# Performance work log

Hardware: AMD Instinct MI355X
Metric: run time of the kernel (lower is better)

Reference implementation:

```python
import jax, jax.numpy as jnp
import numpy as np

NUM_HEADS = 16

def setup_inputs() -> dict:
    key = jax.random.key(0)
    ks = jax.random.split(key, 8)
    B, S, X, D = 2, 2048, 1, 1024
    scale = 1.0 / np.sqrt(D)
    return {
        "query": jax.random.normal(ks[0], (B, S, X, D), jnp.float32),
        "key": jax.random.normal(ks[1], (B, S, X, D), jnp.float32),
        "value": jax.random.normal(ks[2], (B, S, X, D), jnp.float32),
        "Wq": jax.random.normal(ks[3], (D, D), jnp.float32) * scale,
        "bq": jnp.zeros((D,), jnp.float32),
        "Wk": jax.random.normal(ks[4], (D, D), jnp.float32) * scale,
        "bk": jnp.zeros((D,), jnp.float32),
        "Wv": jax.random.normal(ks[5], (D, D), jnp.float32) * scale,
        "bv": jnp.zeros((D,), jnp.float32),
        "Wo": jax.random.normal(ks[6], (D, D), jnp.float32) * scale,
        "bo": jnp.zeros((D,), jnp.float32),
    }

def _split_heads(x, B, H):
    # [B, S, X, D] -> [B, H, S*X, depth]
    D = x.shape[-1]
    return x.reshape(B, -1, H, D // H).transpose(0, 2, 1, 3)

def reference(query, key, value, Wq, bq, Wk, bk, Wv, bv, Wo, bo):
    B, S, X, D = query.shape
    H = NUM_HEADS
    q = _split_heads(query @ Wq + bq, B, H)   # [B,H,L,dh], L=S*X
    k = _split_heads(key @ Wk + bk, B, H)
    v = _split_heads(value @ Wv + bv, B, H)
    dh = k.shape[-1]
    logits = jnp.einsum("bhqd,bhkd->bhqk", q, k) / jnp.sqrt(jnp.float32(dh))
    attn = jax.nn.softmax(logits, axis=-1)
    out = jnp.einsum("bhqk,bhkd->bhqd", attn, v)   # [B,H,L,dh]
    out = out.transpose(0, 2, 1, 3).reshape(B, S, -1, D)  # [B,S,X,D]
    return out @ Wo + bo
```

## Files before the change

### kernel.cpp

```cpp
#include <hip/hip_runtime.h>
#include <cstdint>
#include <cstddef>

typedef __bf16 bf16x8 __attribute__((ext_vector_type(8)));
typedef float f32x4 __attribute__((ext_vector_type(4)));
typedef float f32x16 __attribute__((ext_vector_type(16)));
typedef unsigned short u16;
typedef unsigned int u32;

static constexpr int Bn = 2;
static constexpr int L  = 2048;
static constexpr int Dm = 1024;
static constexpr int H  = 16;
static constexpr int DH = 64;
static constexpr int M  = Bn * L;

#define SC 0.18033688f

__device__ __forceinline__ u16 f2bf(float f) {
    union { float f; u32 u; } v; v.f = f;
    u32 u = v.u + 0x7FFFu + ((v.u >> 16) & 1u);
    return (u16)(u >> 16);
}

__device__ __forceinline__ u32 pk_bf16(float a, float b) {
#if __has_builtin(__builtin_amdgcn_cvt_pk_bf16_f32)
    typedef __bf16 bf16x2_t __attribute__((ext_vector_type(2)));
    bf16x2_t t = __builtin_amdgcn_cvt_pk_bf16_f32(a, b);
    u32 r; __builtin_memcpy(&r, &t, 4); return r;
#else
    return (u32)f2bf(a) | ((u32)f2bf(b) << 16);
#endif
}
__device__ __forceinline__ u16 f2bf1(float f) { return (u16)(pk_bf16(f, f) & 0xffffu); }

__device__ __forceinline__ void gl2lds16(const void* g, void* l) {
    __builtin_amdgcn_global_load_lds(
        (const __attribute__((address_space(1))) u32*)(uintptr_t)g,
        (__attribute__((address_space(3))) u32*)(uintptr_t)l, 16, 0, 0);
}

__global__ __launch_bounds__(256) void convert_in(
    const float* __restrict__ q, const float* __restrict__ k, const float* __restrict__ v,
    u16* __restrict__ dst)
{
    const float* src = (blockIdx.y == 0) ? q : (blockIdx.y == 1) ? k : v;
    u16* d = dst + (size_t)blockIdx.y * M * Dm;
    const size_t t = (size_t)blockIdx.x * 256 + threadIdx.x;
    const float4* s4 = reinterpret_cast<const float4*>(src) + t * 2;
    float4 f0 = s4[0], f1 = s4[1];
    u32 o[4] = { pk_bf16(f0.x, f0.y), pk_bf16(f0.z, f0.w),
                 pk_bf16(f1.x, f1.y), pk_bf16(f1.z, f1.w) };
    reinterpret_cast<uint4*>(d)[t] = *reinterpret_cast<uint4*>(o);
}

__global__ __launch_bounds__(256) void convert_wt(
    const float* __restrict__ Wq, const float* __restrict__ Wk,
    const float* __restrict__ Wv, const float* __restrict__ Wo,
    u16* __restrict__ dst)
{
    __shared__ u16 Ts[64][72];
    const int z = blockIdx.z;
    const float* W = (z == 0) ? Wq : (z == 1) ? Wk : (z == 2) ? Wv : Wo;
    u16* o = dst + (size_t)z * Dm * Dm;
    const int n0 = blockIdx.x * 64, k0 = blockIdx.y * 64;
    const int tid = threadIdx.x;

    {
        const int kr = tid >> 2, nc = (tid & 3) * 16;
        const float* s = W + (size_t)(k0 + kr) * Dm + n0 + nc;
        const float4* s4 = reinterpret_cast<const float4*>(s);
        float4 a = s4[0], b = s4[1], c = s4[2], d = s4[3];
        u32 t[8] = { pk_bf16(a.x, a.y), pk_bf16(a.z, a.w), pk_bf16(b.x, b.y), pk_bf16(b.z, b.w),
                     pk_bf16(c.x, c.y), pk_bf16(c.z, c.w), pk_bf16(d.x, d.y), pk_bf16(d.z, d.w) };
        *reinterpret_cast<uint4*>(&Ts[kr][nc])     = reinterpret_cast<uint4*>(t)[0];
        *reinterpret_cast<uint4*>(&Ts[kr][nc + 8]) = reinterpret_cast<uint4*>(t)[1];
    }
    __syncthreads();
    {
        const int nr = tid >> 2, kc = (tid & 3) * 16;
        u16 w[16];
        #pragma unroll
        for (int j = 0; j < 16; ++j) w[j] = Ts[kc + j][nr];
        u16* dptr = o + (size_t)(n0 + nr) * Dm + k0 + kc;
        *reinterpret_cast<uint4*>(dptr)     = reinterpret_cast<uint4*>(w)[0];
        *reinterpret_cast<uint4*>(dptr + 8) = reinterpret_cast<uint4*>(w)[1];
    }
}

__global__ __launch_bounds__(256) void gemm_qkv(
    const u16* __restrict__ Abuf, const u16* __restrict__ Wtb,
    const float* __restrict__ bq, const float* __restrict__ bk, const float* __restrict__ bv,
    u16* __restrict__ Qh, u16* __restrict__ Kh, u16* __restrict__ Vh)
{
    __shared__ u16 As[2][128 * 32];
    __shared__ u16 Bs[2][128 * 32];
    const int tid = threadIdx.x;
    const int wave = tid >> 6, lane = tid & 63;
    const int quad = lane >> 4, l16 = lane & 15;
    const int wr = wave >> 1, wc = wave & 1;
    const int z = blockIdx.z;
    const u16* A  = Abuf + (size_t)z * M * Dm;
    const u16* Bt = Wtb  + (size_t)z * Dm * Dm;
    const float* bias = (z == 0) ? bq : (z == 1) ? bk : bv;
    u16* out = (z == 0) ? Qh : (z == 1) ? Kh : Vh;
    const int n0 = blockIdx.x * 128, m0 = blockIdx.y * 128;

    const int srow = lane >> 2;
    const int skc  = (lane & 3) * 8;

    f32x4 acc[4][4] = {};

    auto stage = [&](int k0, int bi) {
        #pragma unroll
        for (int i = 0; i < 2; ++i) {
            const int ra = i * 64 + wave * 16;
            gl2lds16(A  + (size_t)(m0 + ra + srow) * Dm + k0 + skc, &As[bi][ra * 32]);
            gl2lds16(Bt + (size_t)(n0 + ra + srow) * Dm + k0 + skc, &Bs[bi][ra * 32]);
        }
    };

    stage(0, 0);
    for (int k0 = 0, it = 0; k0 < Dm; k0 += 32, ++it) {
        const int cb = it & 1;
        __syncthreads();
        if (k0 + 32 < Dm) stage(k0 + 32, cb ^ 1);
        bf16x8 af[4], bf[4];
        #pragma unroll
        for (int t = 0; t < 4; ++t) {
            af[t] = *reinterpret_cast<const bf16x8*>(&As[cb][(wr * 64 + t * 16 + l16) * 32 + quad * 8]);
            bf[t] = *reinterpret_cast<const bf16x8*>(&Bs[cb][(wc * 64 + t * 16 + l16) * 32 + quad * 8]);
        }
        #pragma unroll
        for (int mt = 0; mt < 4; ++mt)
            #pragma unroll
            for (int nt = 0; nt < 4; ++nt)
                acc[mt][nt] = __builtin_amdgcn_mfma_f32_16x16x32_bf16(af[mt], bf[nt], acc[mt][nt], 0, 0, 0);
    }

    const float qscale = (z == 0) ? SC : 1.0f;
    #pragma unroll
    for (int nt = 0; nt < 4; ++nt) {
        const int n = n0 + wc * 64 + nt * 16 + l16;
        const float badd = bias[n];
        const int h = n >> 6, d = n & 63;
        #pragma unroll
        for (int mt = 0; mt < 4; ++mt) {
            #pragma unroll
            for (int r = 0; r < 4; ++r) {
                const int m = m0 + wr * 64 + mt * 16 + quad * 4 + r;
                const int bb = m >> 11, ll = m & 2047;
                out[(((size_t)(bb * H + h)) * L + ll) * DH + d] = f2bf1((acc[mt][nt][r] + badd) * qscale);
            }
        }
    }
}

__global__ __launch_bounds__(256) void transpose_v(
    const u16* __restrict__ Vh, u16* __restrict__ Vth)
{
    __shared__ u16 Ts[64][72];
    const int kt = blockIdx.x, h = blockIdx.y, b = blockIdx.z;
    const int tid = threadIdx.x;
    const size_t hb = ((size_t)(b * H + h)) * L * DH;

    {
        const int kr = tid >> 2, dc = (tid & 3) * 16;
        const u16* s = Vh + hb + (size_t)(kt * 64 + kr) * DH + dc;
        *reinterpret_cast<uint4*>(&Ts[kr][dc])     = *reinterpret_cast<const uint4*>(s);
        *reinterpret_cast<uint4*>(&Ts[kr][dc + 8]) = *reinterpret_cast<const uint4*>(s + 8);
    }
    __syncthreads();
    {
        const int dr = tid >> 2, kc = (tid & 3) * 16;
        u16 w[16];
        #pragma unroll
        for (int j = 0; j < 16; ++j) w[j] = Ts[kc + j][dr];
        u16* dptr = Vth + hb + (size_t)dr * L + kt * 64 + kc;
        *reinterpret_cast<uint4*>(dptr)     = reinterpret_cast<uint4*>(w)[0];
        *reinterpret_cast<uint4*>(dptr + 8) = reinterpret_cast<uint4*>(w)[1];
    }
}

__global__ __launch_bounds__(256) void attn(
    const u16* __restrict__ Qh, const u16* __restrict__ Kh,
    const u16* __restrict__ Vth, u16* __restrict__ ctx)
{
    __shared__ __align__(16) char smem[32768];
    u16* Os = (u16*)smem;

    const int tid  = threadIdx.x;
    const int wave = tid >> 6, lane = tid & 63;
    const int l31  = lane & 31, hh = lane >> 5;
    const int qt = blockIdx.x, h = blockIdx.y, b = blockIdx.z;
    const size_t hb = ((size_t)(b * H + h)) * L * DH;
    const int q0 = qt * 128 + wave * 32;

    bf16x8 qf[4];
    {
        const u16* qp = Qh + hb + (size_t)(q0 + l31) * DH + hh * 8;
        #pragma unroll
        for (int c = 0; c < 4; ++c)
            qf[c] = *reinterpret_cast<const bf16x8*>(qp + c * 16);
    }

    const int r_off = lane >> 3;
    const int s_sl  = lane & 7;

    auto stage = [&](int kt, int bi) {
        char* base = smem + bi * 16384;
        #pragma unroll
        for (int i = 0; i < 2; ++i) {
            const int rr = wave * 16 + i * 8 + r_off;
            gl2lds16(Kh  + hb + (size_t)(kt * 64 + rr) * DH + ((s_sl ^ (rr & 7)) << 3),
                     base + (wave * 16 + i * 8) * 128);
            gl2lds16(Vth + hb + (size_t)rr * L + kt * 64 + ((s_sl ^ (rr & 7)) << 3),
                     base + 8192 + (wave * 16 + i * 8) * 128);
        }
    };

    int vbK[2], vbV[2];
    #pragma unroll
    for (int t = 0; t < 2; ++t) {
        const int rr = t * 32 + l31;
        vbK[t] = rr * 128 + ((rr & 7) << 4);
        vbV[t] = 8192 + rr * 128 + ((rr & 7) << 4);
    }

    float rsum = 0.f;
    f32x16 oacc[2] = {};

    stage(0, 0);
    for (int kt = 0; kt < L / 64; ++kt) {
        const int cb = kt & 1;
        __syncthreads();
        if (kt + 1 < L / 64) stage(kt + 1, cb ^ 1);
        const char* ldsb = smem + cb * 16384;

        f32x16 st[2] = {};
        #pragma unroll
        for (int t = 0; t < 2; ++t) {
            #pragma unroll
            for (int c = 0; c < 4; ++c) {
                bf16x8 kf = *reinterpret_cast<const bf16x8*>(ldsb + (vbK[t] ^ (((c << 1) | hh) << 4)));
                st[t] = __builtin_amdgcn_mfma_f32_32x32x16_bf16(kf, qf[c], st[t], 0, 0, 0);
            }
        }

        bf16x8 pfrag[4];
        #pragma unroll
        for (int t = 0; t < 2; ++t) {
            float p[16];
            #pragma unroll
            for (int rr = 0; rr < 16; ++rr) {
                p[rr] = __builtin_amdgcn_exp2f(st[t][rr]);
                rsum += p[rr];
            }
            #pragma unroll
            for (int g = 0; g < 2; ++g) {
                float* pg = p + g * 8;
                #pragma unroll
                for (int j = 0; j < 4; ++j)
                    asm volatile("v_permlane32_swap_b32 %0, %1" : "+v"(pg[j]), "+v"(pg[j + 4]));
                u32 pkv[4];
                #pragma unroll
                for (int j = 0; j < 4; ++j) pkv[j] = pk_bf16(pg[2 * j], pg[2 * j + 1]);
                pfrag[t * 2 + g] = *reinterpret_cast<bf16x8*>(pkv);
            }
        }

        #pragma unroll
        for (int t = 0; t < 2; ++t) {
            #pragma unroll
            for (int c = 0; c < 4; ++c) {
                bf16x8 vf = *reinterpret_cast<const bf16x8*>(ldsb + (vbV[t] ^ (((c << 1) | hh) << 4)));
                oacc[t] = __builtin_amdgcn_mfma_f32_32x32x16_bf16(vf, pfrag[c], oacc[t], 0, 0, 0);
            }
        }
    }

    rsum += __shfl_xor(rsum, 32);
    const float inv = 1.0f / rsum;

    #pragma unroll
    for (int pass = 0; pass < 2; ++pass) {
        __syncthreads();
        if ((wave >> 1) == pass) {
            const int qloc = (wave & 1) * 32 + l31;
            #pragma unroll
            for (int t = 0; t < 2; ++t) {
                #pragma unroll
                for (int rq = 0; rq < 4; ++rq) {
                    const int d0 = t * 32 + rq * 8 + hh * 4;
                    *reinterpret_cast<u32*>(&Os[qloc * 72 + d0]) =
                        pk_bf16(oacc[t][rq * 4 + 0] * inv, oacc[t][rq * 4 + 1] * inv);
                    *reinterpret_cast<u32*>(&Os[qloc * 72 + d0 + 2]) =
                        pk_bf16(oacc[t][rq * 4 + 2] * inv, oacc[t][rq * 4 + 3] * inv);
                }
            }
        }
        __syncthreads();
        {
            const int row = tid >> 2, cc = (tid & 3) * 16;
            u16* dst = ctx + ((size_t)(b * L + qt * 128 + pass * 64 + row)) * Dm + h * 64 + cc;
            *reinterpret_cast<uint4*>(dst)     = *reinterpret_cast<const uint4*>(&Os[row * 72 + cc]);
            *reinterpret_cast<uint4*>(dst + 8) = *reinterpret_cast<const uint4*>(&Os[row * 72 + cc + 8]);
        }
    }
}

__global__ __launch_bounds__(256) void gemm_out(
    const u16* __restrict__ A, const u16* __restrict__ Bt,
    const float* __restrict__ bias, float* __restrict__ out)
{
    __shared__ u16 As[2][128 * 32];
    __shared__ u16 Bs[2][64 * 32];
    const int tid = threadIdx.x;
    const int wave = tid >> 6, lane = tid & 63;
    const int quad = lane >> 4, l16 = lane & 15;
    const int n0 = blockIdx.x * 64, m0 = blockIdx.y * 128;

    const int srow = lane >> 2;
    const int skc  = (lane & 3) * 8;

    f32x4 acc[2][4] = {};

    auto stage = [&](int k0, int bi) {
        #pragma unroll
        for (int i = 0; i < 2; ++i) {
            const int ra = i * 64 + wave * 16;
            gl2lds16(A + (size_t)(m0 + ra + srow) * Dm + k0 + skc, &As[bi][ra * 32]);
        }
        gl2lds16(Bt + (size_t)(n0 + wave * 16 + srow) * Dm + k0 + skc, &Bs[bi][wave * 16 * 32]);
    };

    stage(0, 0);
    for (int k0 = 0, it = 0; k0 < Dm; k0 += 32, ++it) {
        const int cb = it & 1;
        __syncthreads();
        if (k0 + 32 < Dm) stage(k0 + 32, cb ^ 1);
        bf16x8 af[2], bf[4];
        #pragma unroll
        for (int t = 0; t < 2; ++t)
            af[t] = *reinterpret_cast<const bf16x8*>(&As[cb][(wave * 32 + t * 16 + l16) * 32 + quad * 8]);
        #pragma unroll
        for (int t = 0; t < 4; ++t)
            bf[t] = *reinterpret_cast<const bf16x8*>(&Bs[cb][(t * 16 + l16) * 32 + quad * 8]);
        #pragma unroll
        for (int mt = 0; mt < 2; ++mt)
            #pragma unroll
            for (int nt = 0; nt < 4; ++nt)
                acc[mt][nt] = __builtin_amdgcn_mfma_f32_16x16x32_bf16(af[mt], bf[nt], acc[mt][nt], 0, 0, 0);
    }

    #pragma unroll
    for (int nt = 0; nt < 4; ++nt) {
        const int n = n0 + nt * 16 + l16;
        const float badd = bias[n];
        #pragma unroll
        for (int mt = 0; mt < 2; ++mt) {
            #pragma unroll
            for (int r = 0; r < 4; ++r) {
                const int m = m0 + wave * 32 + mt * 16 + quad * 4 + r;
                out[(size_t)m * Dm + n] = acc[mt][nt][r] + badd;
            }
        }
    }
}

extern "C" void kernel_launch(void* const* d_in, const int* in_sizes, int n_in,
                              void* d_out, int out_size, void* d_ws, size_t ws_size,
                              hipStream_t stream) {
    const float* q  = (const float*)d_in[0];
    const float* k  = (const float*)d_in[1];
    const float* v  = (const float*)d_in[2];
    const float* Wq = (const float*)d_in[3];
    const float* bq = (const float*)d_in[4];
    const float* Wk = (const float*)d_in[5];
    const float* bk = (const float*)d_in[6];
    const float* Wv = (const float*)d_in[7];
    const float* bv = (const float*)d_in[8];
    const float* Wo = (const float*)d_in[9];
    const float* bo = (const float*)d_in[10];
    float* out = (float*)d_out;

    const size_t per = (size_t)Bn * H * L * DH;
    u16* Abuf = (u16*)d_ws;
    u16* Wt   = Abuf + 3 * (size_t)M * Dm;
    u16* Qh   = Wt + 4 * (size_t)Dm * Dm;
    u16* Kh   = Qh + per;
    u16* Vh   = Kh + per;
    u16* Vth  = Vh + per;
    u16* ctx  = Abuf;

    convert_in <<<dim3((M * Dm) / 8 / 256, 3), 256, 0, stream>>>(q, k, v, Abuf);
    convert_wt <<<dim3(Dm / 64, Dm / 64, 4), 256, 0, stream>>>(Wq, Wk, Wv, Wo, Wt);
    gemm_qkv   <<<dim3(Dm / 128, M / 128, 3), 256, 0, stream>>>(Abuf, Wt, bq, bk, bv, Qh, Kh, Vh);
    transpose_v<<<dim3(L / 64, H, Bn), 256, 0, stream>>>(Vh, Vth);
    attn       <<<dim3(L / 128, H, Bn), 256, 0, stream>>>(Qh, Kh, Vth, ctx);
    gemm_out   <<<dim3(Dm / 64, M / 128), 256, 0, stream>>>(ctx, Wt + 3 * (size_t)Dm * Dm, bo, out);
}
```

Measured before the change: 237.8 us.

## Split attention over key halves with merge kernel; fuse V transpose into QKV epilogue

The QKV GEMM epilogue now stages each wave's output tile in shared memory and writes Q/K rows and a transposed V with coalesced 16-byte stores. This removes the separate transpose_v kernel and its extra pass over V. The attention kernel now splits the key range in two, doubling the block count so the GPU is better occupied. Each half writes unnormalized partial outputs and row sums, and a new merge kernel adds the halves and normalizes. The merge costs an extra launch and extra global traffic for the partials. Summing the halves directly is only correct because the softmax does not subtract a running max.

```diff
diff --git a/kernel.cpp b/kernel.cpp
--- a/kernel.cpp
+++ b/kernel.cpp
@@ -14,6 +14,8 @@
 static constexpr int H  = 16;
 static constexpr int DH = 64;
 static constexpr int M  = Bn * L;
+static constexpr size_t PER = (size_t)Bn * H * L * DH;
+static constexpr int NQ = Bn * H * L;
 
 #define SC 0.18033688f
 
@@ -91,10 +93,10 @@
 __global__ __launch_bounds__(256) void gemm_qkv(
     const u16* __restrict__ Abuf, const u16* __restrict__ Wtb,
     const float* __restrict__ bq, const float* __restrict__ bk, const float* __restrict__ bv,
-    u16* __restrict__ Qh, u16* __restrict__ Kh, u16* __restrict__ Vh)
-{
-    __shared__ u16 As[2][128 * 32];
-    __shared__ u16 Bs[2][128 * 32];
+    u16* __restrict__ Qh, u16* __restrict__ Kh, u16* __restrict__ Vth)
+{
+    __shared__ __align__(16) char smem[36864];
+
     const int tid = threadIdx.x;
     const int wave = tid >> 6, lane = tid & 63;
     const int quad = lane >> 4, l16 = lane & 15;
@@ -103,7 +105,7 @@
     const u16* A  = Abuf + (size_t)z * M * Dm;
     const u16* Bt = Wtb  + (size_t)z * Dm * Dm;
     const float* bias = (z == 0) ? bq : (z == 1) ? bk : bv;
-    u16* out = (z == 0) ? Qh : (z == 1) ? Kh : Vh;
+    u16* out = (z == 0) ? Qh : (z == 1) ? Kh : Vth;
     const int n0 = blockIdx.x * 128, m0 = blockIdx.y * 128;
 
     const int srow = lane >> 2;
@@ -115,8 +117,8 @@
         #pragma unroll
         for (int i = 0; i < 2; ++i) {
             const int ra = i * 64 + wave * 16;
-            gl2lds16(A  + (size_t)(m0 + ra + srow) * Dm + k0 + skc, &As[bi][ra * 32]);
-            gl2lds16(Bt + (size_t)(n0 + ra + srow) * Dm + k0 + skc, &Bs[bi][ra * 32]);
+            gl2lds16(A  + (size_t)(m0 + ra + srow) * Dm + k0 + skc, smem + bi * 8192 + ra * 64);
+            gl2lds16(Bt + (size_t)(n0 + ra + srow) * Dm + k0 + skc, smem + 16384 + bi * 8192 + ra * 64);
         }
     };
 
@@ -125,11 +127,13 @@
         const int cb = it & 1;
         __syncthreads();
         if (k0 + 32 < Dm) stage(k0 + 32, cb ^ 1);
+        const u16* Asb = (const u16*)(smem + cb * 8192);
+        const u16* Bsb = (const u16*)(smem + 16384 + cb * 8192);
         bf16x8 af[4], bf[4];
         #pragma unroll
         for (int t = 0; t < 4; ++t) {
-            af[t] = *reinterpret_cast<const bf16x8*>(&As[cb][(wr * 64 + t * 16 + l16) * 32 + quad * 8]);
-            bf[t] = *reinterpret_cast<const bf16x8*>(&Bs[cb][(wc * 64 + t * 16 + l16) * 32 + quad * 8]);
+            af[t] = *reinterpret_cast<const bf16x8*>(&Asb[(wr * 64 + t * 16 + l16) * 32 + quad * 8]);
+            bf[t] = *reinterpret_cast<const bf16x8*>(&Bsb[(wc * 64 + t * 16 + l16) * 32 + quad * 8]);
         }
         #pragma unroll
         for (int mt = 0; mt < 4; ++mt)
@@ -138,53 +142,54 @@
                 acc[mt][nt] = __builtin_amdgcn_mfma_f32_16x16x32_bf16(af[mt], bf[nt], acc[mt][nt], 0, 0, 0);
     }
 
+    __syncthreads();
+    u16* tile = (u16*)smem + wave * 4608;
     const float qscale = (z == 0) ? SC : 1.0f;
     #pragma unroll
     for (int nt = 0; nt < 4; ++nt) {
         const int n = n0 + wc * 64 + nt * 16 + l16;
         const float badd = bias[n];
-        const int h = n >> 6, d = n & 63;
+        const int cc = nt * 16 + l16;
         #pragma unroll
         for (int mt = 0; mt < 4; ++mt) {
             #pragma unroll
             for (int r = 0; r < 4; ++r) {
-                const int m = m0 + wr * 64 + mt * 16 + quad * 4 + r;
-                const int bb = m >> 11, ll = m & 2047;
-                out[(((size_t)(bb * H + h)) * L + ll) * DH + d] = f2bf1((acc[mt][nt][r] + badd) * qscale);
-            }
-        }
-    }
-}
-
-__global__ __launch_bounds__(256) void transpose_v(
-    const u16* __restrict__ Vh, u16* __restrict__ Vth)
-{
-    __shared__ u16 Ts[64][72];
-    const int kt = blockIdx.x, h = blockIdx.y, b = blockIdx.z;
-    const int tid = threadIdx.x;
-    const size_t hb = ((size_t)(b * H + h)) * L * DH;
-
-    {
-        const int kr = tid >> 2, dc = (tid & 3) * 16;
-        const u16* s = Vh + hb + (size_t)(kt * 64 + kr) * DH + dc;
-        *reinterpret_cast<uint4*>(&Ts[kr][dc])     = *reinterpret_cast<const uint4*>(s);
-        *reinterpret_cast<uint4*>(&Ts[kr][dc + 8]) = *reinterpret_cast<const uint4*>(s + 8);
+                const int rr = mt * 16 + quad * 4 + r;
+                const u16 vv = f2bf1((acc[mt][nt][r] + badd) * qscale);
+                if (z == 2) tile[cc * 72 + rr] = vv;
+                else        tile[rr * 72 + cc] = vv;
+            }
+        }
     }
     __syncthreads();
-    {
-        const int dr = tid >> 2, kc = (tid & 3) * 16;
-        u16 w[16];
-        #pragma unroll
-        for (int j = 0; j < 16; ++j) w[j] = Ts[kc + j][dr];
-        u16* dptr = Vth + hb + (size_t)dr * L + kt * 64 + kc;
-        *reinterpret_cast<uint4*>(dptr)     = reinterpret_cast<uint4*>(w)[0];
-        *reinterpret_cast<uint4*>(dptr + 8) = reinterpret_cast<uint4*>(w)[1];
+
+    const int rsub = lane >> 3;
+    const int csub = (lane & 7) * 8;
+    const int h2 = (n0 + wc * 64) >> 6;
+    const int mb = m0 + wr * 64;
+    const int bb = mb >> 11, ll0 = mb & 2047;
+    if (z == 2) {
+        const size_t baseV = ((size_t)(bb * H + h2)) * DH * L;
+        #pragma unroll
+        for (int j = 0; j < 8; ++j) {
+            const int d = j * 8 + rsub;
+            uint4 vv = *reinterpret_cast<const uint4*>(&tile[d * 72 + csub]);
+            *reinterpret_cast<uint4*>(out + baseV + (size_t)d * L + ll0 + csub) = vv;
+        }
+    } else {
+        const size_t base = ((size_t)(bb * H + h2)) * L * DH;
+        #pragma unroll
+        for (int j = 0; j < 8; ++j) {
+            const int row = j * 8 + rsub;
+            uint4 vv = *reinterpret_cast<const uint4*>(&tile[row * 72 + csub]);
+            *reinterpret_cast<uint4*>(out + base + (size_t)(ll0 + row) * DH + csub) = vv;
+        }
     }
 }
 
 __global__ __launch_bounds__(256) void attn(
     const u16* __restrict__ Qh, const u16* __restrict__ Kh,
-    const u16* __restrict__ Vth, u16* __restrict__ ctx)
+    const u16* __restrict__ Vth, u16* __restrict__ Opart, float* __restrict__ rsums)
 {
     __shared__ __align__(16) char smem[32768];
     u16* Os = (u16*)smem;
@@ -192,9 +197,13 @@
     const int tid  = threadIdx.x;
     const int wave = tid >> 6, lane = tid & 63;
     const int l31  = lane & 31, hh = lane >> 5;
-    const int qt = blockIdx.x, h = blockIdx.y, b = blockIdx.z;
+    const int qt = blockIdx.x >> 1, half = blockIdx.x & 1;
+    const int h = blockIdx.y, b = blockIdx.z;
     const size_t hb = ((size_t)(b * H + h)) * L * DH;
     const int q0 = qt * 128 + wave * 32;
+
+    u16*  Op = Opart + (size_t)half * PER;
+    float* rp = rsums + (size_t)half * NQ;
 
     bf16x8 qf[4];
     {
@@ -230,11 +239,12 @@
     float rsum = 0.f;
     f32x16 oacc[2] = {};
 
-    stage(0, 0);
-    for (int kt = 0; kt < L / 64; ++kt) {
-        const int cb = kt & 1;
+    const int kt0 = half * 16;
+    stage(kt0, 0);
+    for (int ktl = 0; ktl < 16; ++ktl) {
+        const int cb = ktl & 1;
         __syncthreads();
-        if (kt + 1 < L / 64) stage(kt + 1, cb ^ 1);
+        if (ktl + 1 < 16) stage(kt0 + ktl + 1, cb ^ 1);
         const char* ldsb = smem + cb * 16384;
 
         f32x16 st[2] = {};
@@ -280,7 +290,6 @@
     }
 
     rsum += __shfl_xor(rsum, 32);
-    const float inv = 1.0f / rsum;
 
     #pragma unroll
     for (int pass = 0; pass < 2; ++pass) {
@@ -293,20 +302,41 @@
                 for (int rq = 0; rq < 4; ++rq) {
                     const int d0 = t * 32 + rq * 8 + hh * 4;
                     *reinterpret_cast<u32*>(&Os[qloc * 72 + d0]) =
-                        pk_bf16(oacc[t][rq * 4 + 0] * inv, oacc[t][rq * 4 + 1] * inv);
+                        pk_bf16(oacc[t][rq * 4 + 0], oacc[t][rq * 4 + 1]);
                     *reinterpret_cast<u32*>(&Os[qloc * 72 + d0 + 2]) =
-                        pk_bf16(oacc[t][rq * 4 + 2] * inv, oacc[t][rq * 4 + 3] * inv);
+                        pk_bf16(oacc[t][rq * 4 + 2], oacc[t][rq * 4 + 3]);
                 }
             }
         }
         __syncthreads();
         {
             const int row = tid >> 2, cc = (tid & 3) * 16;
-            u16* dst = ctx + ((size_t)(b * L + qt * 128 + pass * 64 + row)) * Dm + h * 64 + cc;
+            u16* dst = Op + hb + (size_t)(qt * 128 + pass * 64 + row) * DH + cc;
             *reinterpret_cast<uint4*>(dst)     = *reinterpret_cast<const uint4*>(&Os[row * 72 + cc]);
             *reinterpret_cast<uint4*>(dst + 8) = *reinterpret_cast<const uint4*>(&Os[row * 72 + cc + 8]);
         }
     }
+    if (hh == 0) rp[((size_t)(b * H + h)) * L + q0 + l31] = rsum;
+}
+
+__global__ __launch_bounds__(256) void attn_merge(
+    const u16* __restrict__ O0, const u16* __restrict__ O1,
+    const float* __restrict__ r0, const float* __restrict__ r1,
+    u16* __restrict__ ctx)
+{
+    const int g = blockIdx.x * 256 + threadIdx.x;
+    const int row = g >> 3, dc = (g & 7) * 8;
+    const int b = row >> 15, h = (row >> 11) & (H - 1), l = row & (L - 1);
+    const float inv = 1.0f / (r0[row] + r1[row]);
+    bf16x8 a = *reinterpret_cast<const bf16x8*>(O0 + (size_t)row * DH + dc);
+    bf16x8 c = *reinterpret_cast<const bf16x8*>(O1 + (size_t)row * DH + dc);
+    u32 o[4];
+    #pragma unroll
+    for (int i = 0; i < 4; ++i)
+        o[i] = pk_bf16(((float)a[2 * i] + (float)c[2 * i]) * inv,
+                       ((float)a[2 * i + 1] + (float)c[2 * i + 1]) * inv);
+    *reinterpret_cast<uint4*>(ctx + ((size_t)(b * L + l)) * Dm + h * DH + dc) =
+        *reinterpret_cast<uint4*>(o);
 }
 
 __global__ __launch_bounds__(256) void gemm_out(
@@ -384,19 +414,19 @@
     const float* bo = (const float*)d_in[10];
     float* out = (float*)d_out;
 
-    const size_t per = (size_t)Bn * H * L * DH;
     u16* Abuf = (u16*)d_ws;
     u16* Wt   = Abuf + 3 * (size_t)M * Dm;
     u16* Qh   = Wt + 4 * (size_t)Dm * Dm;
-    u16* Kh   = Qh + per;
-    u16* Vh   = Kh + per;
-    u16* Vth  = Vh + per;
+    u16* Kh   = Qh + PER;
+    u16* Vth  = Kh + PER;
+    u16* O0   = Vth + PER;
+    float* rs = (float*)(O0 + 2 * PER);
     u16* ctx  = Abuf;
 
     convert_in <<<dim3((M * Dm) / 8 / 256, 3), 256, 0, stream>>>(q, k, v, Abuf);
     convert_wt <<<dim3(Dm / 64, Dm / 64, 4), 256, 0, stream>>>(Wq, Wk, Wv, Wo, Wt);
-    gemm_qkv   <<<dim3(Dm / 128, M / 128, 3), 256, 0, stream>>>(Abuf, Wt, bq, bk, bv, Qh, Kh, Vh);
-    transpose_v<<<dim3(L / 64, H, Bn), 256, 0, stream>>>(Vh, Vth);
-    attn       <<<dim3(L / 128, H, Bn), 256, 0, stream>>>(Qh, Kh, Vth, ctx);
+    gemm_qkv   <<<dim3(Dm / 128, M / 128, 3), 256, 0, stream>>>(Abuf, Wt, bq, bk, bv, Qh, Kh, Vth);
+    attn       <<<dim3(L / 128 * 2, H, Bn), 256, 0, stream>>>(Qh, Kh, Vth, O0, rs);
+    attn_merge <<<NQ * 8 / 256, 256, 0, stream>>>(O0, O0 + PER, rs, rs + NQ, ctx);
     gemm_out   <<<dim3(Dm / 64, M / 128), 256, 0, stream>>>(ctx, Wt + 3 * (size_t)Dm * Dm, bo, out);
 }
```

Result: no change. 238.5 us (+0.3%).
